# Performance work log

Hardware: AMD Instinct MI355X
Metric: run time of the kernel (lower is better)

The kernel has to match this reference:

```python
import jax, jax.numpy as jnp
import numpy as np

N_VERTS = 40962   # icosphere level-6 vertices
N_POOL = 10242    # icosphere level-5 vertices (post-pool)
K = 7             # 6 neighbors + self
C1, C2, C3 = 64, 64, 128
IN_CH, OUT_CH = 8, 64
BATCH = 8


def setup_inputs() -> dict:
    key = jax.random.key(0)
    ks = jax.random.split(key, 10)
    x = jax.random.normal(ks[0], (BATCH, IN_CH, N_VERTS), dtype=jnp.float32)
    # neighbor order: 6 random neighbors + self at every 7th slot (as in my_get_neighs_order)
    neb6 = jax.random.randint(ks[1], (N_VERTS, 6), 0, N_VERTS)
    nebs = jnp.concatenate([neb6, jnp.arange(N_VERTS)[:, None]], axis=1).reshape(-1).astype(jnp.int64)
    s1 = 1.0 / np.sqrt(IN_CH)
    s2 = 1.0 / np.sqrt(C1 * K)
    s3 = 1.0 / np.sqrt(C2)
    sf = 1.0 / np.sqrt(C3 * N_POOL)
    W1 = jax.random.uniform(ks[2], (C1, IN_CH), jnp.float32, -s1, s1)
    b1 = jax.random.uniform(ks[3], (C1,), jnp.float32, -s1, s1)
    W2 = jax.random.uniform(ks[4], (C2, C1, K), jnp.float32, -s2, s2)
    b2 = jax.random.uniform(ks[5], (C2,), jnp.float32, -s2, s2)
    W3 = jax.random.uniform(ks[6], (C3, C2), jnp.float32, -s3, s3)
    b3 = jax.random.uniform(ks[7], (C3,), jnp.float32, -s3, s3)
    Wfc = jax.random.uniform(ks[8], (OUT_CH, C3 * N_POOL), jnp.float32, -sf, sf)
    bfc = jax.random.uniform(ks[9], (OUT_CH,), jnp.float32, -sf, sf)
    return {"x": x, "nebs": nebs, "W1": W1, "b1": b1, "W2": W2, "b2": b2,
            "W3": W3, "b3": b3, "Wfc": Wfc, "bfc": bfc}


def reference(x, nebs, W1, b1, W2, b2, W3, b3, Wfc, bfc):
    B = x.shape[0]
    # conv1: 1x1 conv == pointwise matmul over channels
    h1 = jax.nn.relu(jnp.einsum('bci,oc->boi', x, W1) + b1[None, :, None])  # [B,64,N]
    # gather neighbor features, then stride-7 conv collapses the 7 neighbor slots
    g1 = h1[:, :, nebs].reshape(B, C1, N_VERTS, K)                           # [B,64,N,7]
    h2 = jax.nn.relu(jnp.einsum('bcnk,ock->bon', g1, W2) + b2[None, :, None])  # [B,64,N]
    # gather for the first 10242 vertices, maxpool over the 7 neighbor slots
    g2 = h2[:, :, nebs[:N_POOL * K]].reshape(B, C2, N_POOL, K)
    p = jnp.max(g2, axis=-1)                                                  # [B,64,10242]
    # conv3: 1x1 conv
    h3 = jax.nn.relu(jnp.einsum('bci,oc->boi', p, W3) + b3[None, :, None])   # [B,128,10242]
    # dropout is identity in eval mode
    flat = h3.reshape(B, -1)                                                  # [B, 128*10242]
    return flat @ Wfc.T + bfc                                                 # [B, out_ch]
```

## Files before the change

### kernel.cpp

```cpp
#include <hip/hip_runtime.h>

#define NV 40962
#define NP 10242
#define KNB 7
#define C1 64
#define C2 64
#define C3 128
#define INC 8
#define OC 64
#define B 8
#define FCK (C3*NP)
#define NCHUNK (FCK/128)
#define FBLK 1024

typedef __attribute__((ext_vector_type(8))) __bf16 bf16x8;
typedef __attribute__((ext_vector_type(4))) float f32x4;
typedef unsigned short ushort_t;
typedef unsigned int uint_t;

static __device__ __forceinline__ ushort_t f2bf(float f) {
    uint_t u = __float_as_uint(f);
    u = (u + 0x7FFFu + ((u >> 16) & 1u)) >> 16;
    return (ushort_t)u;
}
static __device__ __forceinline__ uint_t pack2(float a, float b) {
    return (uint_t)f2bf(a) | ((uint_t)f2bf(b) << 16);
}

__global__ __launch_bounds__(256) void k_wswz(const float* __restrict__ W2,
        const float* __restrict__ W3, ushort_t* __restrict__ wsw) {
    int idx = blockIdx.x*256 + threadIdx.x;
    if (idx < 28672) {
        int j = idx & 7, lane = (idx >> 3) & 63, rest = idx >> 9;
        int ntile = rest & 3, kstep = rest >> 2;
        int quad = lane >> 4, col = lane & 15;
        int k = kstep*32 + quad*8 + j;
        int o = ntile*16 + col;
        int c = k & 63, knb = k >> 6;
        wsw[idx] = f2bf(W2[(size_t)o*(C1*KNB) + c*KNB + knb]);
    } else if (idx < 28672 + 8192) {
        int s = idx - 28672;
        int j = s & 7, lane = (s >> 3) & 63, rest = s >> 9;
        int ntile = rest & 7, kstep = rest >> 3;
        int quad = lane >> 4, col = lane & 15;
        int c = kstep*32 + quad*8 + j;
        int o3 = ntile*16 + col;
        wsw[idx] = f2bf(W3[(size_t)o3*C2 + c]);
    }
}

__global__ __launch_bounds__(256) void k_conv1(const float* __restrict__ x,
        const float* __restrict__ W1, const float* __restrict__ b1,
        ushort_t* __restrict__ h1bf) {
    __shared__ float sW[C1*INC];
    __shared__ float sb[C1];
    int tid = threadIdx.x;
    for (int i = tid; i < C1*INC; i += 256) sW[i] = W1[i];
    if (tid < C1) sb[tid] = b1[tid];
    __syncthreads();
    long g = (long)blockIdx.x*256 + tid;
    if (g >= (long)NV*B) return;
    int n = (int)(g >> 3);
    int b = (int)(g & 7);
    float xv[INC];
#pragma unroll
    for (int c = 0; c < INC; ++c) xv[c] = x[(size_t)b*INC*NV + (size_t)c*NV + n];
    uint4* outp = (uint4*)(h1bf + ((size_t)n*B + b)*C1);
#pragma unroll
    for (int og = 0; og < 8; ++og) {
        float h[8];
#pragma unroll
        for (int j = 0; j < 8; ++j) {
            int o = og*8 + j;
            float a = sb[o];
#pragma unroll
            for (int c = 0; c < INC; ++c) a += xv[c]*sW[o*INC + c];
            h[j] = fmaxf(a, 0.f);
        }
        uint4 u;
        u.x = pack2(h[0], h[1]); u.y = pack2(h[2], h[3]);
        u.z = pack2(h[4], h[5]); u.w = pack2(h[6], h[7]);
        outp[og] = u;
    }
}

__global__ __launch_bounds__(256) void k_conv2m(const ushort_t* __restrict__ h1bf,
        const int* __restrict__ nebs, const ushort_t* __restrict__ wsw,
        const float* __restrict__ b2, ushort_t* __restrict__ h2bf) {
    int tid = threadIdx.x;
    int wave = tid >> 6, lane = tid & 63;
    int quad = lane >> 4, col = lane & 15;
    int bsub = col & 7;
    int mblock = blockIdx.x * 128;
    int mbase[2];
    int rowt[2][KNB];
    f32x4 acc[2][4];
#pragma unroll
    for (int t = 0; t < 2; ++t) {
        mbase[t] = mblock + wave*32 + t*16;
        int v = (mbase[t] + col) >> 3;
        int vc = v < NV ? v : 0;
#pragma unroll
        for (int kn = 0; kn < KNB; ++kn) rowt[t][kn] = nebs[(size_t)vc*KNB + kn];
#pragma unroll
        for (int nt = 0; nt < 4; ++nt) acc[t][nt] = (f32x4){0.f, 0.f, 0.f, 0.f};
    }
    float bv[4];
#pragma unroll
    for (int nt = 0; nt < 4; ++nt) bv[nt] = b2[nt*16 + col];
    const bf16x8* W = (const bf16x8*)wsw;
#pragma unroll
    for (int ks = 0; ks < 14; ++ks) {
        int knb = ks >> 1;
        int c0 = (ks & 1)*32 + quad*8;
        bf16x8 a0 = *(const bf16x8*)(h1bf + ((size_t)rowt[0][knb]*B + bsub)*C1 + c0);
        bf16x8 a1 = *(const bf16x8*)(h1bf + ((size_t)rowt[1][knb]*B + bsub)*C1 + c0);
#pragma unroll
        for (int nt = 0; nt < 4; ++nt) {
            bf16x8 bf = W[(ks*4 + nt)*64 + lane];
            acc[0][nt] = __builtin_amdgcn_mfma_f32_16x16x32_bf16(a0, bf, acc[0][nt], 0, 0, 0);
            acc[1][nt] = __builtin_amdgcn_mfma_f32_16x16x32_bf16(a1, bf, acc[1][nt], 0, 0, 0);
        }
    }
#pragma unroll
    for (int t = 0; t < 2; ++t) {
#pragma unroll
        for (int r = 0; r < 4; ++r) {
            int m = mbase[t] + quad*4 + r;
            if ((m >> 3) < NV) {
#pragma unroll
                for (int nt = 0; nt < 4; ++nt) {
                    float val = fmaxf(acc[t][nt][r] + bv[nt], 0.f);
                    h2bf[(size_t)m*C2 + nt*16 + col] = f2bf(val);
                }
            }
        }
    }
}

__global__ __launch_bounds__(256) void k_pool(const ushort_t* __restrict__ h2bf,
        const int* __restrict__ nebs, ushort_t* __restrict__ pbf) {
    long t = (long)blockIdx.x*256 + threadIdx.x;
    if (t >= (long)NP*32) return;
    int cg = (int)(t & 3);
    int b  = (int)((t >> 2) & 7);
    int v  = (int)(t >> 5);
    float m[16];
#pragma unroll
    for (int i = 0; i < 16; ++i) m[i] = -1e30f;
    for (int kn = 0; kn < KNB; ++kn) {
        int row = nebs[(size_t)v*KNB + kn];
        const uint4* src = (const uint4*)(h2bf + ((size_t)row*B + b)*C2 + cg*16);
        uint4 u0 = src[0], u1 = src[1];
        uint_t ws[8] = {u0.x, u0.y, u0.z, u0.w, u1.x, u1.y, u1.z, u1.w};
#pragma unroll
        for (int i = 0; i < 8; ++i) {
            float lo = __uint_as_float((ws[i] & 0xFFFFu) << 16);
            float hi = __uint_as_float(ws[i] & 0xFFFF0000u);
            m[2*i]   = fmaxf(m[2*i], lo);
            m[2*i+1] = fmaxf(m[2*i+1], hi);
        }
    }
    uint_t op[8];
#pragma unroll
    for (int i = 0; i < 8; ++i) {
        uint_t lo = __float_as_uint(m[2*i]) >> 16;
        uint_t hi = __float_as_uint(m[2*i+1]) & 0xFFFF0000u;
        op[i] = lo | hi;
    }
    uint4* dst = (uint4*)(pbf + ((size_t)v*B + b)*C2 + cg*16);
    dst[0] = make_uint4(op[0], op[1], op[2], op[3]);
    dst[1] = make_uint4(op[4], op[5], op[6], op[7]);
}

__global__ __launch_bounds__(256) void k_conv3m(const ushort_t* __restrict__ pbf,
        const ushort_t* __restrict__ wsw3, const float* __restrict__ b3,
        float* __restrict__ h3) {
    int tid = threadIdx.x;
    int wave = tid >> 6, lane = tid & 63;
    int quad = lane >> 4, col = lane & 15;
    int m0 = blockIdx.x*64 + wave*16;
    int m = m0 + col;
    int mc = ((m >> 3) < NP) ? m : 0;
    f32x4 acc[8];
#pragma unroll
    for (int nt = 0; nt < 8; ++nt) acc[nt] = (f32x4){0.f, 0.f, 0.f, 0.f};
    float bv[8];
#pragma unroll
    for (int nt = 0; nt < 8; ++nt) bv[nt] = b3[nt*16 + col];
    const bf16x8* W = (const bf16x8*)wsw3;
#pragma unroll
    for (int ks = 0; ks < 2; ++ks) {
        bf16x8 a = *(const bf16x8*)(pbf + (size_t)mc*C2 + ks*32 + quad*8);
#pragma unroll
        for (int nt = 0; nt < 8; ++nt) {
            bf16x8 bf = W[(ks*8 + nt)*64 + lane];
            acc[nt] = __builtin_amdgcn_mfma_f32_16x16x32_bf16(a, bf, acc[nt], 0, 0, 0);
        }
    }
#pragma unroll
    for (int r = 0; r < 4; ++r) {
        int mm = m0 + quad*4 + r;
        int v = mm >> 3, b = mm & 7;
        if (v < NP) {
#pragma unroll
            for (int nt = 0; nt < 8; ++nt) {
                int o3 = nt*16 + col;
                h3[(size_t)b*FCK + (size_t)o3*NP + v] = fmaxf(acc[nt][r] + bv[nt], 0.f);
            }
        }
    }
}

__global__ __launch_bounds__(256) void k_fc(const float* __restrict__ h3,
        const float* __restrict__ Wfc, float* __restrict__ partial) {
    __shared__ float sH[B][128];
    __shared__ float sW[OC][129];
    int tid = threadIdx.x;
    int o = tid & 63;
    int tb = tid >> 6;
    float acc0 = 0.f, acc1 = 0.f;
    for (int ch = blockIdx.x; ch < NCHUNK; ch += FBLK) {
        size_t i0 = (size_t)ch * 128;
        __syncthreads();
        {
            int bb = tid >> 5, i4 = tid & 31;
            float4 f = *(const float4*)(h3 + (size_t)bb*FCK + i0 + i4*4);
            sH[bb][i4*4+0] = f.x; sH[bb][i4*4+1] = f.y;
            sH[bb][i4*4+2] = f.z; sH[bb][i4*4+3] = f.w;
        }
#pragma unroll
        for (int j = 0; j < 8; ++j) {
            int idx = tid + j*256;
            int oo = idx >> 5, i4 = idx & 31;
            float4 f = *(const float4*)(Wfc + (size_t)oo*FCK + i0 + i4*4);
            sW[oo][i4*4+0] = f.x; sW[oo][i4*4+1] = f.y;
            sW[oo][i4*4+2] = f.z; sW[oo][i4*4+3] = f.w;
        }
        __syncthreads();
#pragma unroll 8
        for (int ii = 0; ii < 128; ++ii) {
            float w = sW[o][ii];
            acc0 += w * sH[2*tb][ii];
            acc1 += w * sH[2*tb+1][ii];
        }
    }
    partial[((size_t)blockIdx.x*B + 2*tb  )*OC + o] = acc0;
    partial[((size_t)blockIdx.x*B + 2*tb+1)*OC + o] = acc1;
}

__global__ void k_fcred(const float* __restrict__ partial, const float* __restrict__ bfc,
        float* __restrict__ out) {
    int b = blockIdx.x;
    int o = threadIdx.x;
    float s = 0.f;
    for (int j = 0; j < FBLK; ++j) s += partial[((size_t)j*B + b)*OC + o];
    out[b*OC + o] = s + bfc[o];
}

extern "C" void kernel_launch(void* const* d_in, const int* in_sizes, int n_in,
                              void* d_out, int out_size, void* d_ws, size_t ws_size,
                              hipStream_t stream) {
    const float* x    = (const float*)d_in[0];
    const int*   nebs = (const int*)d_in[1];
    const float* W1   = (const float*)d_in[2];
    const float* b1   = (const float*)d_in[3];
    const float* W2   = (const float*)d_in[4];
    const float* b2   = (const float*)d_in[5];
    const float* W3   = (const float*)d_in[6];
    const float* b3   = (const float*)d_in[7];
    const float* Wfc  = (const float*)d_in[8];
    const float* bfc  = (const float*)d_in[9];
    float* out = (float*)d_out;

    char* ws = (char*)d_ws;
    ushort_t* h1bf = (ushort_t*)(ws);
    ushort_t* h2bf = (ushort_t*)(ws + 42000000);
    ushort_t* pbf  = (ushort_t*)(ws + 84000000);
    float*    h3   = (float*)(ws + 96000000);
    ushort_t* wsw  = (ushort_t*)(ws + 140000000);
    float*    part = (float*)(ws + 141000000);
    ushort_t* wsw3 = wsw + 28672;

    k_wswz<<<144, 256, 0, stream>>>(W2, W3, wsw);
    k_conv1<<<1281, 256, 0, stream>>>(x, W1, b1, h1bf);
    k_conv2m<<<2561, 256, 0, stream>>>(h1bf, nebs, wsw, b2, h2bf);
    k_pool<<<1281, 256, 0, stream>>>(h2bf, nebs, pbf);
    k_conv3m<<<1281, 256, 0, stream>>>(pbf, wsw3, b3, h3);
    k_fc<<<FBLK, 256, 0, stream>>>(h3, Wfc, part);
    k_fcred<<<B, OC, 0, stream>>>(part, bfc, out);
}
```

Before: 635.7 us.

## Fuse maxpool into conv3, merge weight swizzle into conv1, parallelize FC reduce

Merges the weight-swizzle kernel into the conv1 launch as extra blocks and folds the neighbor max-pool directly into the conv3 MFMA kernel. Each lane now gathers 7 neighbor rows and forms its bf16 A fragment in registers instead of reading a pooled intermediate. The final FC reduction uses 256 threads with a shared-memory combine instead of 64 serial threads. This removes two launches and the pooled buffer's write and read round-trip. In exchange, conv3 issues more scattered gather loads per block.

New measurement: 660.5 us. 1.04x slower.

```diff
diff --git a/kernel.cpp b/kernel.cpp
--- a/kernel.cpp
+++ b/kernel.cpp
@@ -27,34 +27,34 @@
     return (uint_t)f2bf(a) | ((uint_t)f2bf(b) << 16);
 }
 
-__global__ __launch_bounds__(256) void k_wswz(const float* __restrict__ W2,
+__global__ __launch_bounds__(256) void k_pre(const float* __restrict__ x,
+        const float* __restrict__ W1, const float* __restrict__ b1,
+        ushort_t* __restrict__ h1bf, const float* __restrict__ W2,
         const float* __restrict__ W3, ushort_t* __restrict__ wsw) {
-    int idx = blockIdx.x*256 + threadIdx.x;
-    if (idx < 28672) {
-        int j = idx & 7, lane = (idx >> 3) & 63, rest = idx >> 9;
-        int ntile = rest & 3, kstep = rest >> 2;
-        int quad = lane >> 4, col = lane & 15;
-        int k = kstep*32 + quad*8 + j;
-        int o = ntile*16 + col;
-        int c = k & 63, knb = k >> 6;
-        wsw[idx] = f2bf(W2[(size_t)o*(C1*KNB) + c*KNB + knb]);
-    } else if (idx < 28672 + 8192) {
-        int s = idx - 28672;
-        int j = s & 7, lane = (s >> 3) & 63, rest = s >> 9;
-        int ntile = rest & 7, kstep = rest >> 3;
-        int quad = lane >> 4, col = lane & 15;
-        int c = kstep*32 + quad*8 + j;
-        int o3 = ntile*16 + col;
-        wsw[idx] = f2bf(W3[(size_t)o3*C2 + c]);
-    }
-}
-
-__global__ __launch_bounds__(256) void k_conv1(const float* __restrict__ x,
-        const float* __restrict__ W1, const float* __restrict__ b1,
-        ushort_t* __restrict__ h1bf) {
     __shared__ float sW[C1*INC];
     __shared__ float sb[C1];
     int tid = threadIdx.x;
+    if (blockIdx.x >= 1281) {
+        int idx = (blockIdx.x - 1281)*256 + tid;
+        if (idx < 28672) {
+            int j = idx & 7, lane = (idx >> 3) & 63, rest = idx >> 9;
+            int ntile = rest & 3, kstep = rest >> 2;
+            int quad = lane >> 4, col = lane & 15;
+            int k = kstep*32 + quad*8 + j;
+            int o = ntile*16 + col;
+            int c = k & 63, knb = k >> 6;
+            wsw[idx] = f2bf(W2[(size_t)o*(C1*KNB) + c*KNB + knb]);
+        } else if (idx < 28672 + 8192) {
+            int s = idx - 28672;
+            int j = s & 7, lane = (s >> 3) & 63, rest = s >> 9;
+            int ntile = rest & 7, kstep = rest >> 3;
+            int quad = lane >> 4, col = lane & 15;
+            int c = kstep*32 + quad*8 + j;
+            int o3 = ntile*16 + col;
+            wsw[idx] = f2bf(W3[(size_t)o3*C2 + c]);
+        }
+        return;
+    }
     for (int i = tid; i < C1*INC; i += 256) sW[i] = W1[i];
     if (tid < C1) sb[tid] = b1[tid];
     __syncthreads();
@@ -138,50 +138,19 @@
     }
 }
 
-__global__ __launch_bounds__(256) void k_pool(const ushort_t* __restrict__ h2bf,
-        const int* __restrict__ nebs, ushort_t* __restrict__ pbf) {
-    long t = (long)blockIdx.x*256 + threadIdx.x;
-    if (t >= (long)NP*32) return;
-    int cg = (int)(t & 3);
-    int b  = (int)((t >> 2) & 7);
-    int v  = (int)(t >> 5);
-    float m[16];
-#pragma unroll
-    for (int i = 0; i < 16; ++i) m[i] = -1e30f;
-    for (int kn = 0; kn < KNB; ++kn) {
-        int row = nebs[(size_t)v*KNB + kn];
-        const uint4* src = (const uint4*)(h2bf + ((size_t)row*B + b)*C2 + cg*16);
-        uint4 u0 = src[0], u1 = src[1];
-        uint_t ws[8] = {u0.x, u0.y, u0.z, u0.w, u1.x, u1.y, u1.z, u1.w};
-#pragma unroll
-        for (int i = 0; i < 8; ++i) {
-            float lo = __uint_as_float((ws[i] & 0xFFFFu) << 16);
-            float hi = __uint_as_float(ws[i] & 0xFFFF0000u);
-            m[2*i]   = fmaxf(m[2*i], lo);
-            m[2*i+1] = fmaxf(m[2*i+1], hi);
-        }
-    }
-    uint_t op[8];
-#pragma unroll
-    for (int i = 0; i < 8; ++i) {
-        uint_t lo = __float_as_uint(m[2*i]) >> 16;
-        uint_t hi = __float_as_uint(m[2*i+1]) & 0xFFFF0000u;
-        op[i] = lo | hi;
-    }
-    uint4* dst = (uint4*)(pbf + ((size_t)v*B + b)*C2 + cg*16);
-    dst[0] = make_uint4(op[0], op[1], op[2], op[3]);
-    dst[1] = make_uint4(op[4], op[5], op[6], op[7]);
-}
-
-__global__ __launch_bounds__(256) void k_conv3m(const ushort_t* __restrict__ pbf,
-        const ushort_t* __restrict__ wsw3, const float* __restrict__ b3,
-        float* __restrict__ h3) {
+__global__ __launch_bounds__(256) void k_poolconv3(const ushort_t* __restrict__ h2bf,
+        const int* __restrict__ nebs, const ushort_t* __restrict__ wsw3,
+        const float* __restrict__ b3, float* __restrict__ h3) {
     int tid = threadIdx.x;
     int wave = tid >> 6, lane = tid & 63;
     int quad = lane >> 4, col = lane & 15;
     int m0 = blockIdx.x*64 + wave*16;
     int m = m0 + col;
     int mc = ((m >> 3) < NP) ? m : 0;
+    int v = mc >> 3, bsub = mc & 7;
+    int rowt[KNB];
+#pragma unroll
+    for (int kn = 0; kn < KNB; ++kn) rowt[kn] = nebs[(size_t)v*KNB + kn];
     f32x4 acc[8];
 #pragma unroll
     for (int nt = 0; nt < 8; ++nt) acc[nt] = (f32x4){0.f, 0.f, 0.f, 0.f};
@@ -191,7 +160,28 @@
     const bf16x8* W = (const bf16x8*)wsw3;
 #pragma unroll
     for (int ks = 0; ks < 2; ++ks) {
-        bf16x8 a = *(const bf16x8*)(pbf + (size_t)mc*C2 + ks*32 + quad*8);
+        float mx[8];
+#pragma unroll
+        for (int i = 0; i < 8; ++i) mx[i] = -1e30f;
+#pragma unroll
+        for (int kn = 0; kn < KNB; ++kn) {
+            uint4 u = *(const uint4*)(h2bf + ((size_t)rowt[kn]*B + bsub)*C2 + ks*32 + quad*8);
+            uint_t ws[4] = {u.x, u.y, u.z, u.w};
+#pragma unroll
+            for (int i = 0; i < 4; ++i) {
+                float lo = __uint_as_float((ws[i] & 0xFFFFu) << 16);
+                float hi = __uint_as_float(ws[i] & 0xFFFF0000u);
+                mx[2*i]   = fmaxf(mx[2*i], lo);
+                mx[2*i+1] = fmaxf(mx[2*i+1], hi);
+            }
+        }
+        uint4 pk;
+        pk.x = (__float_as_uint(mx[0]) >> 16) | (__float_as_uint(mx[1]) & 0xFFFF0000u);
+        pk.y = (__float_as_uint(mx[2]) >> 16) | (__float_as_uint(mx[3]) & 0xFFFF0000u);
+        pk.z = (__float_as_uint(mx[4]) >> 16) | (__float_as_uint(mx[5]) & 0xFFFF0000u);
+        pk.w = (__float_as_uint(mx[6]) >> 16) | (__float_as_uint(mx[7]) & 0xFFFF0000u);
+        bf16x8 a;
+        __builtin_memcpy(&a, &pk, 16);
 #pragma unroll
         for (int nt = 0; nt < 8; ++nt) {
             bf16x8 bf = W[(ks*8 + nt)*64 + lane];
@@ -201,12 +191,12 @@
 #pragma unroll
     for (int r = 0; r < 4; ++r) {
         int mm = m0 + quad*4 + r;
-        int v = mm >> 3, b = mm & 7;
-        if (v < NP) {
+        int vv = mm >> 3, b = mm & 7;
+        if (vv < NP) {
 #pragma unroll
             for (int nt = 0; nt < 8; ++nt) {
                 int o3 = nt*16 + col;
-                h3[(size_t)b*FCK + (size_t)o3*NP + v] = fmaxf(acc[nt][r] + bv[nt], 0.f);
+                h3[(size_t)b*FCK + (size_t)o3*NP + vv] = fmaxf(acc[nt][r] + bv[nt], 0.f);
             }
         }
     }
@@ -249,13 +239,16 @@
     partial[((size_t)blockIdx.x*B + 2*tb+1)*OC + o] = acc1;
 }
 
-__global__ void k_fcred(const float* __restrict__ partial, const float* __restrict__ bfc,
-        float* __restrict__ out) {
+__global__ __launch_bounds__(256) void k_fcred(const float* __restrict__ partial,
+        const float* __restrict__ bfc, float* __restrict__ out) {
+    __shared__ float red[4][64];
     int b = blockIdx.x;
-    int o = threadIdx.x;
+    int o = threadIdx.x & 63, jg = threadIdx.x >> 6;
     float s = 0.f;
-    for (int j = 0; j < FBLK; ++j) s += partial[((size_t)j*B + b)*OC + o];
-    out[b*OC + o] = s + bfc[o];
+    for (int j = jg; j < FBLK; j += 4) s += partial[((size_t)j*B + b)*OC + o];
+    red[jg][o] = s;
+    __syncthreads();
+    if (jg == 0) out[b*OC + o] = red[0][o] + red[1][o] + red[2][o] + red[3][o] + bfc[o];
 }
 
 extern "C" void kernel_launch(void* const* d_in, const int* in_sizes, int n_in,
@@ -276,17 +269,14 @@
     char* ws = (char*)d_ws;
     ushort_t* h1bf = (ushort_t*)(ws);
     ushort_t* h2bf = (ushort_t*)(ws + 42000000);
-    ushort_t* pbf  = (ushort_t*)(ws + 84000000);
     float*    h3   = (float*)(ws + 96000000);
     ushort_t* wsw  = (ushort_t*)(ws + 140000000);
     float*    part = (float*)(ws + 141000000);
     ushort_t* wsw3 = wsw + 28672;
 
-    k_wswz<<<144, 256, 0, stream>>>(W2, W3, wsw);
-    k_conv1<<<1281, 256, 0, stream>>>(x, W1, b1, h1bf);
+    k_pre<<<1425, 256, 0, stream>>>(x, W1, b1, h1bf, W2, W3, wsw);
     k_conv2m<<<2561, 256, 0, stream>>>(h1bf, nebs, wsw, b2, h2bf);
-    k_pool<<<1281, 256, 0, stream>>>(h2bf, nebs, pbf);
-    k_conv3m<<<1281, 256, 0, stream>>>(pbf, wsw3, b3, h3);
+    k_poolconv3<<<1281, 256, 0, stream>>>(h2bf, nebs, wsw3, b3, h3);
     k_fc<<<FBLK, 256, 0, stream>>>(h3, Wfc, part);
-    k_fcred<<<B, OC, 0, stream>>>(part, bfc, out);
-}
+    k_fcred<<<B, 256, 0, stream>>>(part, bfc, out);
+}
```
